# Optimization experiments

Hardware: AMD Instinct MI355X
Metric: run time of the kernel (lower is better)

## Reference

```python
import jax, jax.numpy as jnp
import numpy as np

N = 100_000            # particles
E = 3_200_000          # edges (avg degree 32)
DIM = 3
H = 1.0                # kernel_radius
SIGMA = 3.0 / 359.0 / np.pi / H**3   # 3D quintic kernel normalization
RHO_REF = 1.0
P_REF = 100.0          # rho_ref * (10*u_ref)**2 / gamma, gamma=1
P_BG = 0.0             # p_bg_factor * p_ref
ETA0 = 0.01            # base_viscosity
EPS = 1e-8


def _qpows(d, p):
    q = d / H
    return (jnp.maximum(0.0, 1.0 - q) ** p,
            jnp.maximum(0.0, 2.0 - q) ** p,
            jnp.maximum(0.0, 3.0 - q) ** p)


def kernel_w(d):
    q1, q2, q3 = _qpows(d, 5)
    return SIGMA * (q3 - 6.0 * q2 + 15.0 * q1)


def kernel_grad_w(d):
    q1, q2, q3 = _qpows(d, 4)
    return (SIGMA / H) * (-5.0 * q3 + 30.0 * q2 - 75.0 * q1)


def setup_inputs() -> dict:
    key = jax.random.key(0)
    k1, k2, k3, k4 = jax.random.split(key, 4)
    r = jax.random.uniform(k1, (N, DIM), dtype=jnp.float32)   # positions in unit box
    v = jax.random.normal(k2, (N, DIM), dtype=jnp.float32)    # velocity history (last frame)
    i_s = jax.random.randint(k3, (E,), 0, N)                  # receivers
    j_s = jax.random.randint(k4, (E,), 0, N)                  # senders
    return {"r": r, "v": v, "i_s": i_s, "j_s": j_s}


def reference(r, v, i_s, j_s):
    n = r.shape[0]
    # --- per-edge gather + kernel ---
    dr = r[i_s] - r[j_s]                       # displacement_fn, [E,3]
    d = jnp.sqrt(jnp.sum(dr * dr, axis=-1))    # [E]
    w = kernel_w(d)
    # --- density summation (scatter) ---
    mass = jnp.ones((n,), r.dtype)
    rho = mass * jax.ops.segment_sum(w, i_s, num_segments=n)
    # Tait EoS, gamma=1
    p = P_REF * (rho / RHO_REF - 1.0) + P_BG
    eta = jnp.full((n,), ETA0, r.dtype)

    # --- per-edge acceleration (gather particle fields to edges) ---
    rho_i, rho_j = rho[i_s], rho[j_s]
    p_i, p_j = p[i_s], p[j_s]
    eta_i, eta_j = eta[i_s], eta[j_s]
    u_i, u_j = v[i_s], v[j_s]                  # u == v in _transform
    v_i, v_j = u_i, u_j

    eta_ij = 2.0 * eta_i * eta_j / (eta_i + eta_j + EPS)
    p_ij = (rho_j * p_i + rho_i * p_j) / (rho_i + rho_j)
    # ((m_i/rho_i)^2 + (m_j/rho_j)^2)/m_i with m == 1
    wvol = (1.0 / rho_i) ** 2 + (1.0 / rho_j) ** 2
    c = wvol * kernel_grad_w(d) / (d + EPS)    # [E]

    # transport stress A = (outer(rho_i*u_i, v_i-u_i) + outer(rho_j*u_j, v_j-u_j))/2, [E,3,3]
    A = 0.5 * (rho_i[:, None, None] * u_i[:, :, None] * (v_i - u_i)[:, None, :]
               + rho_j[:, None, None] * u_j[:, :, None] * (v_j - u_j)[:, None, :])
    Ar = jnp.einsum('eij,ej->ei', A, dr)

    a_eq_8 = c[:, None] * (-p_ij[:, None] * dr + Ar + eta_ij[:, None] * (u_i - u_j))
    p_bg_i = jnp.zeros_like(p_i)               # _transform passes zeros
    a_eq_13 = (c * p_bg_i)[:, None] * dr

    # --- scatter-reduce to particles ---
    dudt = jax.ops.segment_sum(a_eq_8, i_s, num_segments=n)   # [N,3]
    dvdt = jax.ops.segment_sum(a_eq_13, i_s, num_segments=n)  # [N,3]

    # pack state outputs: [rho, p, dudt(3), dvdt(3)] -> [N,8]
    return jnp.concatenate([rho[:, None], p[:, None], dudt, dvdt], axis=1)
```

## Files before the change

kernel.cpp:

```cpp
#include <hip/hip_runtime.h>
#include <math.h>

#ifndef M_PI
#define M_PI 3.14159265358979323846
#endif

static constexpr float kSigma = (float)(3.0 / 359.0 / M_PI);
static constexpr float kPRef  = 100.0f;
static constexpr float kEps   = 1e-8f;
static constexpr float kEta   = (float)(2.0 * 0.01 * 0.01 / (0.01 + 0.01 + 1e-8));
static constexpr float kInvQ  = 1.0f / 65536.0f;

#define CH     4096
#define SL_SH  12
#define SLICE  4096
#define IB_SH  9
#define IBSZ   512
#define C2MAX  48
#define NSUB2  4
#define PB     512
#define BATP   4

typedef _Float16 hf4 __attribute__((ext_vector_type(4)));

__device__ __forceinline__ float pow5f(float t) { float t2 = t * t; return t2 * t2 * t; }
__device__ __forceinline__ float pow4f(float t) { float t2 = t * t; return t2 * t2; }

__device__ __forceinline__ int nt_load_i(const int* p) { return __builtin_nontemporal_load(p); }
__device__ __forceinline__ hf4 nt_load_h4(const hf4* p) { return __builtin_nontemporal_load(p); }
__device__ __forceinline__ void nt_store_h4(hf4* p, hf4 v) { __builtin_nontemporal_store(v, p); }

__device__ __forceinline__ int scanned(const int* __restrict__ gscan,
                                       const int* __restrict__ bscan, int idx) {
    return gscan[idx] + bscan[idx >> 8];
}

__global__ void k_pack_pos(const float* __restrict__ r, ushort4* __restrict__ posq,
                           float* __restrict__ rho, float* __restrict__ acc, int n) {
    int i = blockIdx.x * blockDim.x + threadIdx.x;
    if (i >= n) return;
    float x = r[3 * i], y = r[3 * i + 1], z = r[3 * i + 2];
    ushort4 q;
    q.x = (unsigned short)fminf(x * 65536.0f, 65535.0f);
    q.y = (unsigned short)fminf(y * 65536.0f, 65535.0f);
    q.z = (unsigned short)fminf(z * 65536.0f, 65535.0f);
    q.w = 0;
    posq[i] = q;
    rho[i] = 0.f;
    acc[3 * i] = 0.f; acc[3 * i + 1] = 0.f; acc[3 * i + 2] = 0.f;
}

__global__ void k_hist1(const int* __restrict__ i_s, int* __restrict__ ghist,
                        int nbA, int nsl, int E) {
    __shared__ int h[64];
    int t = threadIdx.x, blk = blockIdx.x;
    if (t < 64) h[t] = 0;
    __syncthreads();
    int base = blk * CH;
    int end = min(base + CH, E);
    for (int kb = base; kb < end; kb += 256 * 4) {
        int iv[4];
#pragma unroll
        for (int b = 0; b < 4; b++) {
            int k = kb + b * 256 + t;
            iv[b] = (k < end) ? i_s[k] : -1;
        }
#pragma unroll
        for (int b = 0; b < 4; b++)
            if (iv[b] >= 0) atomicAdd(&h[iv[b] >> SL_SH], 1);
    }
    __syncthreads();
    if (t < nsl) ghist[t * nbA + blk] = h[t];
}

__global__ void k_scan_block(const int* __restrict__ in, int* __restrict__ out,
                             int* __restrict__ bsum, int m) {
    __shared__ int s[256];
    int t = threadIdx.x;
    int i = blockIdx.x * 256 + t;
    int x = (i < m) ? in[i] : 0;
    s[t] = x;
    __syncthreads();
    for (int d = 1; d < 256; d <<= 1) {
        int v = (t >= d) ? s[t - d] : 0;
        __syncthreads();
        s[t] += v;
        __syncthreads();
    }
    if (i < m) out[i] = s[t] - x;
    if (t == 255) bsum[blockIdx.x] = s[255];
}

__global__ void k_scan_bsums(const int* __restrict__ bsum, int* __restrict__ bscan, int nb) {
    __shared__ int s[512];
    __shared__ int carry;
    int t = threadIdx.x;
    if (t == 0) carry = 0;
    __syncthreads();
    for (int base = 0; base < nb; base += 512) {
        int i = base + t;
        int x = (i < nb) ? bsum[i] : 0;
        s[t] = x;
        __syncthreads();
        for (int d = 1; d < 512; d <<= 1) {
            int v = (t >= d) ? s[t - d] : 0;
            __syncthreads();
            s[t] += v;
            __syncthreads();
        }
        if (i < nb) bscan[i] = s[t] - x + carry;
        __syncthreads();
        if (t == 511) carry += s[511];
        __syncthreads();
    }
}

__global__ void k_split1(const int* __restrict__ i_s, const int* __restrict__ j_s,
                         const int* __restrict__ ghist, const int* __restrict__ gscan,
                         const int* __restrict__ bscan, int* __restrict__ pairs1,
                         int nbA, int nsl, int E) {
    __shared__ int lofs[64];
    __shared__ int ldelta[64];
    __shared__ int stage[CH];
    __shared__ unsigned short binof[CH];
    int t = threadIdx.x, blk = blockIdx.x;
    int base = blk * CH;
    int end = min(base + CH, E);
    int cnt = end - base;

    if (t < 64) {
        int h0 = (t < nsl) ? ghist[t * nbA + blk] : 0;
        lofs[t] = h0;
    }
    __syncthreads();
    if (t == 0) {
        int run = 0;
        for (int b = 0; b < nsl; b++) {
            int h = lofs[b];
            lofs[b] = run;
            ldelta[b] = scanned(gscan, bscan, b * nbA + blk) - run;
            run += h;
        }
    }
    __syncthreads();

    for (int kb = base; kb < end; kb += 256 * 4) {
        int iv[4], jv[4];
#pragma unroll
        for (int b = 0; b < 4; b++) {
            int k = kb + b * 256 + t;
            iv[b] = (k < end) ? i_s[k] : -1;
            jv[b] = (k < end) ? j_s[k] : 0;
        }
#pragma unroll
        for (int b = 0; b < 4; b++) {
            if (iv[b] < 0) continue;
            int bin = iv[b] >> SL_SH;
            int pos = atomicAdd(&lofs[bin], 1);
            stage[pos] = (jv[b] << SL_SH) | (iv[b] & (SLICE - 1));
            binof[pos] = (unsigned short)bin;
        }
    }
    __syncthreads();
    for (int x = t; x < cnt; x += 256)
        pairs1[x + ldelta[binof[x]]] = stage[x];
}

__device__ __forceinline__ int key2_of(int pv) {
    return (((pv >> IB_SH) & 7) << 5) | (pv >> 24);
}

__global__ void k_hist2(const int* __restrict__ pairs1, const int* __restrict__ gscan1,
                        const int* __restrict__ bscan1, int* __restrict__ ghist2,
                        int nbA, int nsl, int E) {
    __shared__ int h[256];
    int t = threadIdx.x;
    int s = blockIdx.x / C2MAX, c = blockIdx.x % C2MAX;
    h[t] = 0;
    __syncthreads();
    int start = scanned(gscan1, bscan1, s * nbA);
    int end = (s + 1 < nsl) ? scanned(gscan1, bscan1, (s + 1) * nbA) : E;
    int a0 = start + c * CH, a1 = min(a0 + CH, end);
    for (int kb = a0; kb < a1; kb += 256 * 4) {
        int pv[4];
#pragma unroll
        for (int b = 0; b < 4; b++) {
            int k = kb + b * 256 + t;
            pv[b] = (k < a1) ? pairs1[k] : -1;
        }
#pragma unroll
        for (int b = 0; b < 4; b++)
            if (pv[b] >= 0) atomicAdd(&h[key2_of(pv[b])], 1);
    }
    __syncthreads();
    ghist2[(s * 256 + t) * C2MAX + c] = h[t];
}

__global__ void k_split2(const int* __restrict__ pairs1, const int* __restrict__ ghist2,
                         const int* __restrict__ gscan2, const int* __restrict__ bscan2,
                         const int* __restrict__ gscan1, const int* __restrict__ bscan1,
                         int* __restrict__ pairs2, int nbA, int nsl, int E) {
    __shared__ int lofs[256];
    __shared__ int ldelta[256];
    __shared__ int stage[CH];
    __shared__ unsigned short binof[CH];
    int t = threadIdx.x;
    int s = blockIdx.x / C2MAX, c = blockIdx.x % C2MAX;
    int start = scanned(gscan1, bscan1, s * nbA);
    int end = (s + 1 < nsl) ? scanned(gscan1, bscan1, (s + 1) * nbA) : E;
    int a0 = start + c * CH, a1 = min(a0 + CH, end);
    int cnt = max(a1 - a0, 0);

    int h0 = ghist2[(s * 256 + t) * C2MAX + c];
    lofs[t] = h0;
    __syncthreads();
    for (int d = 1; d < 256; d <<= 1) {
        int v = (t >= d) ? lofs[t - d] : 0;
        __syncthreads();
        lofs[t] += v;
        __syncthreads();
    }
    int e0 = lofs[t] - h0;
    __syncthreads();
    lofs[t] = e0;
    ldelta[t] = scanned(gscan2, bscan2, (s * 256 + t) * C2MAX + c) - e0;
    __syncthreads();

    for (int kb = a0; kb < a1; kb += 256 * 4) {
        int pv[4];
#pragma unroll
        for (int b = 0; b < 4; b++) {
            int k = kb + b * 256 + t;
            pv[b] = (k < a1) ? pairs1[k] : -1;
        }
#pragma unroll
        for (int b = 0; b < 4; b++) {
            if (pv[b] < 0) continue;
            int bin = key2_of(pv[b]);
            int pos = atomicAdd(&lofs[bin], 1);
            stage[pos] = pv[b];
            binof[pos] = (unsigned short)bin;
        }
    }
    __syncthreads();
    for (int x = t; x < cnt; x += 256)
        pairs2[x + ldelta[binof[x]]] = stage[x];
}

__device__ __forceinline__ void bin_range(const int* __restrict__ gscan2,
                                          const int* __restrict__ bscan2,
                                          int bin, int nk2, int E, int t, int* sse) {
    int islice = bin >> 3, ibin_in = bin & 7;
    int lin = (islice * 256 + (ibin_in << 5)) * C2MAX;
    int lin1 = lin + 32 * C2MAX;
    if (t == 0) sse[0] = scanned(gscan2, bscan2, lin);
    if (t == 1) sse[1] = (lin1 < nk2) ? scanned(gscan2, bscan2, lin1) : E;
}

__global__ void __launch_bounds__(PB, 8)
k_pass1(const ushort4* __restrict__ posq, const int* __restrict__ pairs2,
        const int* __restrict__ gscan2, const int* __restrict__ bscan2,
        float* __restrict__ rho, hf4* __restrict__ aux,
        int n, int E, int nk2) {
    __shared__ ushort4 sip[IBSZ];
    __shared__ float srho[IBSZ];
    __shared__ int sse[2];
    int t = threadIdx.x;
    int bin = blockIdx.x / NSUB2, sub = blockIdx.x % NSUB2;
    int i0 = bin << IB_SH;
    {
        int ig = i0 + t;
        sip[t] = (ig < n) ? posq[ig] : make_ushort4(0, 0, 0, 0);
        srho[t] = 0.f;
    }
    bin_range(gscan2, bscan2, bin, nk2, E, t, sse);
    __syncthreads();
    int ks = sse[0], len = sse[1] - sse[0];
    int k0 = ks + (int)((long)len * sub / NSUB2);
    int k1 = ks + (int)((long)len * (sub + 1) / NSUB2);
    for (int kb = k0; kb < k1; kb += PB * BATP) {
        int pr[BATP], kk[BATP];
        bool live[BATP];
#pragma unroll
        for (int b = 0; b < BATP; b++) {
            int k = kb + b * PB + t;
            live[b] = (k < k1);
            kk[b] = live[b] ? k : k1 - 1;
            pr[b] = nt_load_i(&pairs2[kk[b]]);
        }
        ushort4 pj[BATP], pi[BATP];
#pragma unroll
        for (int b = 0; b < BATP; b++) {
            pj[b] = posq[pr[b] >> SL_SH];
            pi[b] = sip[pr[b] & (IBSZ - 1)];
        }
#pragma unroll
        for (int b = 0; b < BATP; b++) {
            float dx = (float)((int)pi[b].x - (int)pj[b].x) * kInvQ;
            float dy = (float)((int)pi[b].y - (int)pj[b].y) * kInvQ;
            float dz = (float)((int)pi[b].z - (int)pj[b].z) * kInvQ;
            float d = sqrtf(dx * dx + dy * dy + dz * dz);
            float t1 = fmaxf(1.f - d, 0.f);
            float t2 = fmaxf(2.f - d, 0.f);
            float t3 = fmaxf(3.f - d, 0.f);
            float w = kSigma * (pow5f(t3) - 6.f * pow5f(t2) + 15.f * pow5f(t1));
            hf4 h;
            h.x = (_Float16)dx; h.y = (_Float16)dy;
            h.z = (_Float16)dz; h.w = (_Float16)d;
            if (live[b]) {
                atomicAdd(&srho[pr[b] & (IBSZ - 1)], w);
                nt_store_h4(&aux[kk[b]], h);
            }
        }
    }
    __syncthreads();
    {
        int ig = i0 + t;
        if (ig < n && srho[t] != 0.f) atomicAdd(&rho[ig], srho[t]);
    }
}

__global__ void k_mid(const float* __restrict__ rho, const float* __restrict__ v,
                      hf4* __restrict__ vpq, float* __restrict__ out, int n) {
    int i = blockIdx.x * blockDim.x + threadIdx.x;
    if (i >= n) return;
    float rh = rho[i];
    float pp = kPRef * (rh - 1.0f);
    hf4 h;
    h.x = (_Float16)v[3 * i];
    h.y = (_Float16)v[3 * i + 1];
    h.z = (_Float16)v[3 * i + 2];
    h.w = (_Float16)pp;
    vpq[i] = h;
    float* o = out + (size_t)i * 8;
    o[0] = rh;
    o[1] = pp;
    o[5] = 0.f; o[6] = 0.f; o[7] = 0.f;
}

__global__ void __launch_bounds__(PB, 8)
k_pass2(const hf4* __restrict__ vpq, const int* __restrict__ pairs2,
        const hf4* __restrict__ aux, const int* __restrict__ gscan2,
        const int* __restrict__ bscan2, float* __restrict__ acc,
        int n, int E, int nk2) {
    __shared__ hf4 siv[IBSZ];
    __shared__ float sax[IBSZ], say[IBSZ], saz[IBSZ];
    __shared__ int sse[2];
    int t = threadIdx.x;
    int bin = blockIdx.x / NSUB2, sub = blockIdx.x % NSUB2;
    int i0 = bin << IB_SH;
    {
        int ig = i0 + t;
        siv[t] = (ig < n) ? vpq[ig] : hf4{0, 0, 0, 0};
        sax[t] = 0.f; say[t] = 0.f; saz[t] = 0.f;
    }
    bin_range(gscan2, bscan2, bin, nk2, E, t, sse);
    __syncthreads();
    int ks = sse[0], len = sse[1] - sse[0];
    int k0 = ks + (int)((long)len * sub / NSUB2);
    int k1 = ks + (int)((long)len * (sub + 1) / NSUB2);
    for (int kb = k0; kb < k1; kb += PB * BATP) {
        int pr[BATP], kk[BATP];
        bool live[BATP];
        hf4 hx[BATP];
#pragma unroll
        for (int b = 0; b < BATP; b++) {
            int k = kb + b * PB + t;
            live[b] = (k < k1);
            kk[b] = live[b] ? k : k1 - 1;
            pr[b] = nt_load_i(&pairs2[kk[b]]);
            hx[b] = nt_load_h4(&aux[kk[b]]);
        }
        hf4 vj[BATP], vi[BATP];
#pragma unroll
        for (int b = 0; b < BATP; b++) {
            vj[b] = vpq[pr[b] >> SL_SH];
            vi[b] = siv[pr[b] & (IBSZ - 1)];
        }
#pragma unroll
        for (int b = 0; b < BATP; b++) {
            int il = pr[b] & (IBSZ - 1);
            float dx = (float)hx[b].x, dy = (float)hx[b].y, dz = (float)hx[b].z;
            float d = (float)hx[b].w;
            float p_i = (float)vi[b].w, p_j = (float)vj[b].w;
            float rho_i = p_i * 0.01f + 1.0f;
            float rho_j = p_j * 0.01f + 1.0f;
            float t1 = fmaxf(1.f - d, 0.f);
            float t2 = fmaxf(2.f - d, 0.f);
            float t3 = fmaxf(3.f - d, 0.f);
            float gw = kSigma * (-5.f * pow4f(t3) + 30.f * pow4f(t2) - 75.f * pow4f(t1));
            float inv_i = 1.0f / rho_i, inv_j = 1.0f / rho_j;
            float c = (inv_i * inv_i + inv_j * inv_j) * gw / (d + kEps);
            float p_ij = (rho_j * p_i + rho_i * p_j) / (rho_i + rho_j);
            if (live[b]) {
                atomicAdd(&sax[il], c * (kEta * ((float)vi[b].x - (float)vj[b].x) - p_ij * dx));
                atomicAdd(&say[il], c * (kEta * ((float)vi[b].y - (float)vj[b].y) - p_ij * dy));
                atomicAdd(&saz[il], c * (kEta * ((float)vi[b].z - (float)vj[b].z) - p_ij * dz));
            }
        }
    }
    __syncthreads();
    {
        int ig = i0 + t;
        if (ig < n) {
            if (sax[t] != 0.f) atomicAdd(&acc[3 * ig],     sax[t]);
            if (say[t] != 0.f) atomicAdd(&acc[3 * ig + 1], say[t]);
            if (saz[t] != 0.f) atomicAdd(&acc[3 * ig + 2], saz[t]);
        }
    }
}

__global__ void k_fin(const float* __restrict__ acc, float* __restrict__ out, int n) {
    int i = blockIdx.x * blockDim.x + threadIdx.x;
    if (i >= n) return;
    float* o = out + (size_t)i * 8 + 2;
    o[0] = acc[3 * i];
    o[1] = acc[3 * i + 1];
    o[2] = acc[3 * i + 2];
}

static inline char* wcarve(char*& ws, size_t bytes) {
    char* p = ws;
    ws += (bytes + 255) & ~(size_t)255;
    return p;
}

extern "C" void kernel_launch(void* const* d_in, const int* in_sizes, int n_in,
                              void* d_out, int out_size, void* d_ws, size_t ws_size,
                              hipStream_t stream) {
    const float* r = (const float*)d_in[0];
    const float* v = (const float*)d_in[1];
    const int* i_s = (const int*)d_in[2];
    const int* j_s = (const int*)d_in[3];
    int n = in_sizes[0] / 3;
    int E = in_sizes[2];
    float* out = (float*)d_out;

    int nsl  = ((n - 1) >> SL_SH) + 1;
    int nbin = ((n - 1) >> IB_SH) + 1;
    int nk2  = nsl * 256 * C2MAX;
    int nbA  = (E + CH - 1) / CH;
    int m1   = nsl * nbA;
    int m2   = nk2;
    int nb1  = (m1 + 255) / 256;
    int nb2  = (m2 + 255) / 256;

    char* ws = (char*)d_ws;
    ushort4* posq   = (ushort4*)wcarve(ws, (size_t)n * 8);
    hf4*     vpq    = (hf4*)wcarve(ws, (size_t)n * 8);
    float*   rho    = (float*)wcarve(ws, (size_t)n * 4);
    float*   acc    = (float*)wcarve(ws, (size_t)n * 12);
    int*     ghist1 = (int*)wcarve(ws, (size_t)m1 * 4);
    int*     gscan1 = (int*)wcarve(ws, (size_t)m1 * 4);
    int*     bsum1  = (int*)wcarve(ws, (size_t)nb1 * 4);
    int*     bscan1 = (int*)wcarve(ws, (size_t)nb1 * 4);
    int*     pairs1 = (int*)wcarve(ws, (size_t)E * 4);
    int*     ghist2 = (int*)wcarve(ws, (size_t)m2 * 4);
    int*     gscan2 = (int*)wcarve(ws, (size_t)m2 * 4);
    int*     bsum2  = (int*)wcarve(ws, (size_t)nb2 * 4);
    int*     bscan2 = (int*)wcarve(ws, (size_t)nb2 * 4);
    int*     pairs2 = (int*)wcarve(ws, (size_t)E * 4);
    hf4*     aux    = (hf4*)wcarve(ws, (size_t)E * 8);

    const int bs = 256;
    int gn = (n + bs - 1) / bs;

    k_pack_pos<<<gn, bs, 0, stream>>>(r, posq, rho, acc, n);
    k_hist1<<<nbA, 256, 0, stream>>>(i_s, ghist1, nbA, nsl, E);
    k_scan_block<<<nb1, 256, 0, stream>>>(ghist1, gscan1, bsum1, m1);
    k_scan_bsums<<<1, 512, 0, stream>>>(bsum1, bscan1, nb1);
    k_split1<<<nbA, 256, 0, stream>>>(i_s, j_s, ghist1, gscan1, bscan1, pairs1, nbA, nsl, E);
    k_hist2<<<nsl * C2MAX, 256, 0, stream>>>(pairs1, gscan1, bscan1, ghist2, nbA, nsl, E);
    k_scan_block<<<nb2, 256, 0, stream>>>(ghist2, gscan2, bsum2, m2);
    k_scan_bsums<<<1, 512, 0, stream>>>(bsum2, bscan2, nb2);
    k_split2<<<nsl * C2MAX, 256, 0, stream>>>(pairs1, ghist2, gscan2, bscan2,
                                              gscan1, bscan1, pairs2, nbA, nsl, E);
    k_pass1<<<nbin * NSUB2, PB, 0, stream>>>(posq, pairs2, gscan2, bscan2, rho, aux,
                                             n, E, nk2);
    k_mid<<<gn, bs, 0, stream>>>(rho, v, vpq, out, n);
    k_pass2<<<nbin * NSUB2, PB, 0, stream>>>(vpq, pairs2, aux, gscan2, bscan2, acc,
                                             n, E, nk2);
    k_fin<<<gn, bs, 0, stream>>>(acc, out, n);
}
```

Before: 228.7 us.

## Pack velocity with positions and refine sender binning for gather locality

Velocity is packed as fp16 next to the quantized position in one 16-byte per-particle record, and pass1 computes the velocity-difference term, storing it in a wider 16-byte per-edge aux record. Pass2 then gathers only a 4-byte pressure value per sender instead of an 8-byte vector. The second radix sort key grows from 32 to 256 sender buckets (2048 keys), so edges within a receiver bin are ordered by finer sender blocks to improve gather cache locality. In exchange the per-edge aux traffic doubles, the histogram and scan arrays grow eightfold, and split2 needs a per-thread multi-bucket scan.

Measured after the change: 313.1 us. 36.9% more time.

```diff
diff --git a/kernel.cpp b/kernel.cpp
--- a/kernel.cpp
+++ b/kernel.cpp
@@ -16,36 +16,56 @@
 #define SLICE  4096
 #define IB_SH  9
 #define IBSZ   512
+#define JB_SH  9
+#define KEY2N  2048
 #define C2MAX  48
 #define NSUB2  4
 #define PB     512
 #define BATP   4
 
-typedef _Float16 hf4 __attribute__((ext_vector_type(4)));
+typedef unsigned int uv4 __attribute__((ext_vector_type(4)));
 
 __device__ __forceinline__ float pow5f(float t) { float t2 = t * t; return t2 * t2 * t; }
 __device__ __forceinline__ float pow4f(float t) { float t2 = t * t; return t2 * t2; }
 
 __device__ __forceinline__ int nt_load_i(const int* p) { return __builtin_nontemporal_load(p); }
-__device__ __forceinline__ hf4 nt_load_h4(const hf4* p) { return __builtin_nontemporal_load(p); }
-__device__ __forceinline__ void nt_store_h4(hf4* p, hf4 v) { __builtin_nontemporal_store(v, p); }
+__device__ __forceinline__ uint4 nt_load_u4(const uint4* p) {
+    uv4 v = __builtin_nontemporal_load((const uv4*)p);
+    return make_uint4(v[0], v[1], v[2], v[3]);
+}
+__device__ __forceinline__ void nt_store_u4(uint4* p, uint4 v) {
+    uv4 t = {v.x, v.y, v.z, v.w};
+    __builtin_nontemporal_store(t, (uv4*)p);
+}
+
+__device__ __forceinline__ float f16tof(unsigned int bits) {
+    _Float16 h; unsigned short b = (unsigned short)bits;
+    __builtin_memcpy(&h, &b, 2); return (float)h;
+}
+__device__ __forceinline__ unsigned int ftof16(float f) {
+    _Float16 h = (_Float16)f; unsigned short b;
+    __builtin_memcpy(&b, &h, 2); return (unsigned int)b;
+}
 
 __device__ __forceinline__ int scanned(const int* __restrict__ gscan,
                                        const int* __restrict__ bscan, int idx) {
     return gscan[idx] + bscan[idx >> 8];
 }
 
-__global__ void k_pack_pos(const float* __restrict__ r, ushort4* __restrict__ posq,
-                           float* __restrict__ rho, float* __restrict__ acc, int n) {
+__global__ void k_pack(const float* __restrict__ r, const float* __restrict__ v,
+                       uint4* __restrict__ pvq, float* __restrict__ rho,
+                       float* __restrict__ acc, int n) {
     int i = blockIdx.x * blockDim.x + threadIdx.x;
     if (i >= n) return;
-    float x = r[3 * i], y = r[3 * i + 1], z = r[3 * i + 2];
-    ushort4 q;
-    q.x = (unsigned short)fminf(x * 65536.0f, 65535.0f);
-    q.y = (unsigned short)fminf(y * 65536.0f, 65535.0f);
-    q.z = (unsigned short)fminf(z * 65536.0f, 65535.0f);
+    unsigned qx = (unsigned)fminf(r[3 * i] * 65536.0f, 65535.0f);
+    unsigned qy = (unsigned)fminf(r[3 * i + 1] * 65536.0f, 65535.0f);
+    unsigned qz = (unsigned)fminf(r[3 * i + 2] * 65536.0f, 65535.0f);
+    uint4 q;
+    q.x = qx | (qy << 16);
+    q.y = qz | (ftof16(v[3 * i]) << 16);
+    q.z = ftof16(v[3 * i + 1]) | (ftof16(v[3 * i + 2]) << 16);
     q.w = 0;
-    posq[i] = q;
+    pvq[i] = q;
     rho[i] = 0.f;
     acc[3 * i] = 0.f; acc[3 * i + 1] = 0.f; acc[3 * i + 2] = 0.f;
 }
@@ -167,16 +187,16 @@
 }
 
 __device__ __forceinline__ int key2_of(int pv) {
-    return (((pv >> IB_SH) & 7) << 5) | (pv >> 24);
+    return (((pv >> IB_SH) & 7) << 8) | (pv >> (SL_SH + JB_SH));
 }
 
 __global__ void k_hist2(const int* __restrict__ pairs1, const int* __restrict__ gscan1,
                         const int* __restrict__ bscan1, int* __restrict__ ghist2,
                         int nbA, int nsl, int E) {
-    __shared__ int h[256];
+    __shared__ int h[KEY2N];
     int t = threadIdx.x;
     int s = blockIdx.x / C2MAX, c = blockIdx.x % C2MAX;
-    h[t] = 0;
+    for (int q = t; q < KEY2N; q += 256) h[q] = 0;
     __syncthreads();
     int start = scanned(gscan1, bscan1, s * nbA);
     int end = (s + 1 < nsl) ? scanned(gscan1, bscan1, (s + 1) * nbA) : E;
@@ -193,15 +213,17 @@
             if (pv[b] >= 0) atomicAdd(&h[key2_of(pv[b])], 1);
     }
     __syncthreads();
-    ghist2[(s * 256 + t) * C2MAX + c] = h[t];
+    for (int q = t; q < KEY2N; q += 256)
+        ghist2[((size_t)s * KEY2N + q) * C2MAX + c] = h[q];
 }
 
 __global__ void k_split2(const int* __restrict__ pairs1, const int* __restrict__ ghist2,
                          const int* __restrict__ gscan2, const int* __restrict__ bscan2,
                          const int* __restrict__ gscan1, const int* __restrict__ bscan1,
                          int* __restrict__ pairs2, int nbA, int nsl, int E) {
-    __shared__ int lofs[256];
-    __shared__ int ldelta[256];
+    __shared__ int lofs[KEY2N];
+    __shared__ int ldelta[KEY2N];
+    __shared__ int stot[256];
     __shared__ int stage[CH];
     __shared__ unsigned short binof[CH];
     int t = threadIdx.x;
@@ -211,19 +233,32 @@
     int a0 = start + c * CH, a1 = min(a0 + CH, end);
     int cnt = max(a1 - a0, 0);
 
-    int h0 = ghist2[(s * 256 + t) * C2MAX + c];
-    lofs[t] = h0;
+    const int Q = KEY2N / 256;
+    int hq[Q];
+    int run = 0;
+#pragma unroll
+    for (int q = 0; q < Q; q++) {
+        int e = t * Q + q;
+        hq[q] = ghist2[((size_t)s * KEY2N + e) * C2MAX + c];
+        lofs[e] = run;
+        run += hq[q];
+    }
+    stot[t] = run;
     __syncthreads();
     for (int d = 1; d < 256; d <<= 1) {
-        int v = (t >= d) ? lofs[t - d] : 0;
-        __syncthreads();
-        lofs[t] += v;
-        __syncthreads();
-    }
-    int e0 = lofs[t] - h0;
-    __syncthreads();
-    lofs[t] = e0;
-    ldelta[t] = scanned(gscan2, bscan2, (s * 256 + t) * C2MAX + c) - e0;
+        int v = (t >= d) ? stot[t - d] : 0;
+        __syncthreads();
+        stot[t] += v;
+        __syncthreads();
+    }
+    int base2 = stot[t] - run;
+#pragma unroll
+    for (int q = 0; q < Q; q++) {
+        int e = t * Q + q;
+        int excl = base2 + lofs[e];
+        lofs[e] = excl;
+        ldelta[e] = scanned(gscan2, bscan2, ((size_t)s * KEY2N + e) * C2MAX + c) - excl;
+    }
     __syncthreads();
 
     for (int kb = a0; kb < a1; kb += 256 * 4) {
@@ -249,20 +284,20 @@
 
 __device__ __forceinline__ void bin_range(const int* __restrict__ gscan2,
                                           const int* __restrict__ bscan2,
-                                          int bin, int nk2, int E, int t, int* sse) {
+                                          int bin, long nk2, int E, int t, int* sse) {
     int islice = bin >> 3, ibin_in = bin & 7;
-    int lin = (islice * 256 + (ibin_in << 5)) * C2MAX;
-    int lin1 = lin + 32 * C2MAX;
-    if (t == 0) sse[0] = scanned(gscan2, bscan2, lin);
-    if (t == 1) sse[1] = (lin1 < nk2) ? scanned(gscan2, bscan2, lin1) : E;
+    long lin = ((long)islice * KEY2N + (ibin_in << 8)) * C2MAX;
+    long lin1 = lin + (long)256 * C2MAX;
+    if (t == 0) sse[0] = scanned(gscan2, bscan2, (int)lin);
+    if (t == 1) sse[1] = (lin1 < nk2) ? scanned(gscan2, bscan2, (int)lin1) : E;
 }
 
 __global__ void __launch_bounds__(PB, 8)
-k_pass1(const ushort4* __restrict__ posq, const int* __restrict__ pairs2,
+k_pass1(const uint4* __restrict__ pvq, const int* __restrict__ pairs2,
         const int* __restrict__ gscan2, const int* __restrict__ bscan2,
-        float* __restrict__ rho, hf4* __restrict__ aux,
-        int n, int E, int nk2) {
-    __shared__ ushort4 sip[IBSZ];
+        float* __restrict__ rho, uint4* __restrict__ aux,
+        int n, int E, long nk2) {
+    __shared__ uint4 sipv[IBSZ];
     __shared__ float srho[IBSZ];
     __shared__ int sse[2];
     int t = threadIdx.x;
@@ -270,7 +305,7 @@
     int i0 = bin << IB_SH;
     {
         int ig = i0 + t;
-        sip[t] = (ig < n) ? posq[ig] : make_ushort4(0, 0, 0, 0);
+        sipv[t] = (ig < n) ? pvq[ig] : make_uint4(0, 0, 0, 0);
         srho[t] = 0.f;
     }
     bin_range(gscan2, bscan2, bin, nk2, E, t, sse);
@@ -288,28 +323,33 @@
             kk[b] = live[b] ? k : k1 - 1;
             pr[b] = nt_load_i(&pairs2[kk[b]]);
         }
-        ushort4 pj[BATP], pi[BATP];
+        uint4 qj[BATP], qi[BATP];
 #pragma unroll
         for (int b = 0; b < BATP; b++) {
-            pj[b] = posq[pr[b] >> SL_SH];
-            pi[b] = sip[pr[b] & (IBSZ - 1)];
+            qj[b] = pvq[pr[b] >> SL_SH];
+            qi[b] = sipv[pr[b] & (IBSZ - 1)];
         }
 #pragma unroll
         for (int b = 0; b < BATP; b++) {
-            float dx = (float)((int)pi[b].x - (int)pj[b].x) * kInvQ;
-            float dy = (float)((int)pi[b].y - (int)pj[b].y) * kInvQ;
-            float dz = (float)((int)pi[b].z - (int)pj[b].z) * kInvQ;
+            float dx = (float)((int)(qi[b].x & 0xffff) - (int)(qj[b].x & 0xffff)) * kInvQ;
+            float dy = (float)((int)(qi[b].x >> 16)    - (int)(qj[b].x >> 16))    * kInvQ;
+            float dz = (float)((int)(qi[b].y & 0xffff) - (int)(qj[b].y & 0xffff)) * kInvQ;
             float d = sqrtf(dx * dx + dy * dy + dz * dz);
             float t1 = fmaxf(1.f - d, 0.f);
             float t2 = fmaxf(2.f - d, 0.f);
             float t3 = fmaxf(3.f - d, 0.f);
             float w = kSigma * (pow5f(t3) - 6.f * pow5f(t2) + 15.f * pow5f(t1));
-            hf4 h;
-            h.x = (_Float16)dx; h.y = (_Float16)dy;
-            h.z = (_Float16)dz; h.w = (_Float16)d;
+            float gx = kEta * (f16tof(qi[b].y >> 16) - f16tof(qj[b].y >> 16));
+            float gy = kEta * (f16tof(qi[b].z)       - f16tof(qj[b].z));
+            float gz = kEta * (f16tof(qi[b].z >> 16) - f16tof(qj[b].z >> 16));
+            uint4 a;
+            a.x = ftof16(dx) | (ftof16(dy) << 16);
+            a.y = ftof16(dz) | (ftof16(d) << 16);
+            a.z = ftof16(gx) | (ftof16(gy) << 16);
+            a.w = ftof16(gz);
             if (live[b]) {
                 atomicAdd(&srho[pr[b] & (IBSZ - 1)], w);
-                nt_store_h4(&aux[kk[b]], h);
+                nt_store_u4(&aux[kk[b]], a);
             }
         }
     }
@@ -320,18 +360,13 @@
     }
 }
 
-__global__ void k_mid(const float* __restrict__ rho, const float* __restrict__ v,
-                      hf4* __restrict__ vpq, float* __restrict__ out, int n) {
+__global__ void k_mid(const float* __restrict__ rho, float* __restrict__ p,
+                      float* __restrict__ out, int n) {
     int i = blockIdx.x * blockDim.x + threadIdx.x;
     if (i >= n) return;
     float rh = rho[i];
     float pp = kPRef * (rh - 1.0f);
-    hf4 h;
-    h.x = (_Float16)v[3 * i];
-    h.y = (_Float16)v[3 * i + 1];
-    h.z = (_Float16)v[3 * i + 2];
-    h.w = (_Float16)pp;
-    vpq[i] = h;
+    p[i] = pp;
     float* o = out + (size_t)i * 8;
     o[0] = rh;
     o[1] = pp;
@@ -339,11 +374,11 @@
 }
 
 __global__ void __launch_bounds__(PB, 8)
-k_pass2(const hf4* __restrict__ vpq, const int* __restrict__ pairs2,
-        const hf4* __restrict__ aux, const int* __restrict__ gscan2,
+k_pass2(const float* __restrict__ p, const int* __restrict__ pairs2,
+        const uint4* __restrict__ aux, const int* __restrict__ gscan2,
         const int* __restrict__ bscan2, float* __restrict__ acc,
-        int n, int E, int nk2) {
-    __shared__ hf4 siv[IBSZ];
+        int n, int E, long nk2) {
+    __shared__ float sp[IBSZ];
     __shared__ float sax[IBSZ], say[IBSZ], saz[IBSZ];
     __shared__ int sse[2];
     int t = threadIdx.x;
@@ -351,7 +386,7 @@
     int i0 = bin << IB_SH;
     {
         int ig = i0 + t;
-        siv[t] = (ig < n) ? vpq[ig] : hf4{0, 0, 0, 0};
+        sp[t] = (ig < n) ? p[ig] : 0.f;
         sax[t] = 0.f; say[t] = 0.f; saz[t] = 0.f;
     }
     bin_range(gscan2, bscan2, bin, nk2, E, t, sse);
@@ -362,27 +397,29 @@
     for (int kb = k0; kb < k1; kb += PB * BATP) {
         int pr[BATP], kk[BATP];
         bool live[BATP];
-        hf4 hx[BATP];
+        uint4 ax[BATP];
 #pragma unroll
         for (int b = 0; b < BATP; b++) {
             int k = kb + b * PB + t;
             live[b] = (k < k1);
             kk[b] = live[b] ? k : k1 - 1;
             pr[b] = nt_load_i(&pairs2[kk[b]]);
-            hx[b] = nt_load_h4(&aux[kk[b]]);
-        }
-        hf4 vj[BATP], vi[BATP];
+            ax[b] = nt_load_u4(&aux[kk[b]]);
+        }
+        float pj[BATP], pi[BATP];
 #pragma unroll
         for (int b = 0; b < BATP; b++) {
-            vj[b] = vpq[pr[b] >> SL_SH];
-            vi[b] = siv[pr[b] & (IBSZ - 1)];
+            pj[b] = p[pr[b] >> SL_SH];
+            pi[b] = sp[pr[b] & (IBSZ - 1)];
         }
 #pragma unroll
         for (int b = 0; b < BATP; b++) {
             int il = pr[b] & (IBSZ - 1);
-            float dx = (float)hx[b].x, dy = (float)hx[b].y, dz = (float)hx[b].z;
-            float d = (float)hx[b].w;
-            float p_i = (float)vi[b].w, p_j = (float)vj[b].w;
+            float dx = f16tof(ax[b].x), dy = f16tof(ax[b].x >> 16);
+            float dz = f16tof(ax[b].y), d  = f16tof(ax[b].y >> 16);
+            float gx = f16tof(ax[b].z), gy = f16tof(ax[b].z >> 16);
+            float gz = f16tof(ax[b].w);
+            float p_i = pi[b], p_j = pj[b];
             float rho_i = p_i * 0.01f + 1.0f;
             float rho_j = p_j * 0.01f + 1.0f;
             float t1 = fmaxf(1.f - d, 0.f);
@@ -393,9 +430,9 @@
             float c = (inv_i * inv_i + inv_j * inv_j) * gw / (d + kEps);
             float p_ij = (rho_j * p_i + rho_i * p_j) / (rho_i + rho_j);
             if (live[b]) {
-                atomicAdd(&sax[il], c * (kEta * ((float)vi[b].x - (float)vj[b].x) - p_ij * dx));
-                atomicAdd(&say[il], c * (kEta * ((float)vi[b].y - (float)vj[b].y) - p_ij * dy));
-                atomicAdd(&saz[il], c * (kEta * ((float)vi[b].z - (float)vj[b].z) - p_ij * dz));
+                atomicAdd(&sax[il], c * (gx - p_ij * dx));
+                atomicAdd(&say[il], c * (gy - p_ij * dy));
+                atomicAdd(&saz[il], c * (gz - p_ij * dz));
             }
         }
     }
@@ -438,17 +475,17 @@
 
     int nsl  = ((n - 1) >> SL_SH) + 1;
     int nbin = ((n - 1) >> IB_SH) + 1;
-    int nk2  = nsl * 256 * C2MAX;
+    long nk2 = (long)nsl * KEY2N * C2MAX;
     int nbA  = (E + CH - 1) / CH;
     int m1   = nsl * nbA;
-    int m2   = nk2;
+    int m2   = (int)nk2;
     int nb1  = (m1 + 255) / 256;
     int nb2  = (m2 + 255) / 256;
 
     char* ws = (char*)d_ws;
-    ushort4* posq   = (ushort4*)wcarve(ws, (size_t)n * 8);
-    hf4*     vpq    = (hf4*)wcarve(ws, (size_t)n * 8);
+    uint4*   pvq    = (uint4*)wcarve(ws, (size_t)n * 16);
     float*   rho    = (float*)wcarve(ws, (size_t)n * 4);
+    float*   p      = (float*)wcarve(ws, (size_t)n * 4);
     float*   acc    = (float*)wcarve(ws, (size_t)n * 12);
     int*     ghist1 = (int*)wcarve(ws, (size_t)m1 * 4);
     int*     gscan1 = (int*)wcarve(ws, (size_t)m1 * 4);
@@ -460,12 +497,12 @@
     int*     bsum2  = (int*)wcarve(ws, (size_t)nb2 * 4);
     int*     bscan2 = (int*)wcarve(ws, (size_t)nb2 * 4);
     int*     pairs2 = (int*)wcarve(ws, (size_t)E * 4);
-    hf4*     aux    = (hf4*)wcarve(ws, (size_t)E * 8);
+    uint4*   aux    = (uint4*)wcarve(ws, (size_t)E * 16);
 
     const int bs = 256;
     int gn = (n + bs - 1) / bs;
 
-    k_pack_pos<<<gn, bs, 0, stream>>>(r, posq, rho, acc, n);
+    k_pack<<<gn, bs, 0, stream>>>(r, v, pvq, rho, acc, n);
     k_hist1<<<nbA, 256, 0, stream>>>(i_s, ghist1, nbA, nsl, E);
     k_scan_block<<<nb1, 256, 0, stream>>>(ghist1, gscan1, bsum1, m1);
     k_scan_bsums<<<1, 512, 0, stream>>>(bsum1, bscan1, nb1);
@@ -475,10 +512,10 @@
     k_scan_bsums<<<1, 512, 0, stream>>>(bsum2, bscan2, nb2);
     k_split2<<<nsl * C2MAX, 256, 0, stream>>>(pairs1, ghist2, gscan2, bscan2,
                                               gscan1, bscan1, pairs2, nbA, nsl, E);
-    k_pass1<<<nbin * NSUB2, PB, 0, stream>>>(posq, pairs2, gscan2, bscan2, rho, aux,
+    k_pass1<<<nbin * NSUB2, PB, 0, stream>>>(pvq, pairs2, gscan2, bscan2, rho, aux,
                                              n, E, nk2);
-    k_mid<<<gn, bs, 0, stream>>>(rho, v, vpq, out, n);
-    k_pass2<<<nbin * NSUB2, PB, 0, stream>>>(vpq, pairs2, aux, gscan2, bscan2, acc,
+    k_mid<<<gn, bs, 0, stream>>>(rho, p, out, n);
+    k_pass2<<<nbin * NSUB2, PB, 0, stream>>>(p, pairs2, aux, gscan2, bscan2, acc,
                                              n, E, nk2);
     k_fin<<<gn, bs, 0, stream>>>(acc, out, n);
 }
```
